# Optimization experiments

Measured on AMD Instinct MI355X. Metric: run time of the kernel, lower is better.

The kernel has to match this reference:

```python
import jax, jax.numpy as jnp
import numpy as np

D_MODEL = 768
HEAD_SIZE = 64

def setup_inputs() -> dict:
    key = jax.random.key(0)
    ks = jax.random.split(key, 7)
    B, S = 8, 2048
    x = jax.random.normal(ks[0], (B, S, D_MODEL), dtype=jnp.float32)
    s = 1.0 / np.sqrt(D_MODEL)
    Wq = jax.random.uniform(ks[1], (D_MODEL, HEAD_SIZE), jnp.float32, -s, s)
    bq = jnp.zeros((HEAD_SIZE,), jnp.float32)
    Wk = jax.random.uniform(ks[2], (D_MODEL, HEAD_SIZE), jnp.float32, -s, s)
    bk = jnp.zeros((HEAD_SIZE,), jnp.float32)
    Wv = jax.random.uniform(ks[3], (D_MODEL, HEAD_SIZE), jnp.float32, -s, s)
    bv = jnp.zeros((HEAD_SIZE,), jnp.float32)
    return {"x": x, "Wq": Wq, "bq": bq, "Wk": Wk, "bk": bk, "Wv": Wv, "bv": bv}

def reference(x, Wq, bq, Wk, bk, Wv, bv):
    # Single attention head: softmax(Q K^T / sqrt(head_size)) V
    q = jnp.einsum('bsd,dh->bsh', x, Wq) + bq  # [B,S,H]
    k = jnp.einsum('bsd,dh->bsh', x, Wk) + bk
    v = jnp.einsum('bsd,dh->bsh', x, Wv) + bv
    scale = 1.0 / jnp.sqrt(jnp.array(HEAD_SIZE, dtype=x.dtype))
    scores = jnp.einsum('bqh,bkh->bqk', q, k) * scale  # [B,S,S]
    attn = jax.nn.softmax(scores, axis=-1)
    out = jnp.einsum('bqk,bkh->bqh', attn, v)  # [B,S,H]
    return out
```

## Files before the change

kernel.cpp:

```cpp
#include <hip/hip_runtime.h>
#include <math.h>

#define D_MODEL 768
#define HS 64
#define BATCH 8
#define SEQ 2048
#define SCALE 0.125f
#define KSPLIT 8
#define KCHUNK (SEQ / KSPLIT)
#define PM 32

typedef _Float16 half_t;
typedef __attribute__((ext_vector_type(8))) _Float16 half8;
typedef __attribute__((ext_vector_type(4))) float floatx4;

typedef const __attribute__((address_space(1))) void gas_void;
typedef __attribute__((address_space(3))) void las_void;
__device__ __forceinline__ void gl_lds16(const void* g, void* l) {
    __builtin_amdgcn_global_load_lds((gas_void*)g, (las_void*)l, 16, 0, 0);
}
__device__ __forceinline__ void waitcnt_all() {
    __builtin_amdgcn_s_waitcnt(0);
}

__global__ __launch_bounds__(256)
void wconv_kernel(const float* __restrict__ Wq, const float* __restrict__ Wk,
                  const float* __restrict__ Wv, half_t* __restrict__ Wt)
{
    int m = blockIdx.x >> 6;
    int h = blockIdx.x & 63;
    const float* W = (m == 0) ? Wq : ((m == 1) ? Wk : Wv);
    half_t* dst = Wt + (size_t)blockIdx.x * D_MODEL;
    for (int k = threadIdx.x; k < D_MODEL; k += 256)
        dst[k] = (half_t)W[(size_t)k * HS + h];
}

__global__ __launch_bounds__(256)
void proj_kernel(const float* __restrict__ x, const half_t* __restrict__ Wt,
                 const float* __restrict__ bq, const float* __restrict__ bk,
                 const float* __restrict__ bv,
                 half_t* __restrict__ Qh, half_t* __restrict__ Kh,
                 half_t* __restrict__ Vt)
{
    __shared__ __align__(16) half_t xs[2][PM * 64];
    __shared__ __align__(16) half_t wt[2][192 * 64];

    const int tid = threadIdx.x;
    const int w = tid >> 6;
    const int lane = tid & 63;
    const int l15 = lane & 15;
    const int quad = lane >> 4;
    const long row0 = (long)blockIdx.x * PM;

    floatx4 acc[2][3];
#pragma unroll
    for (int i = 0; i < 2; ++i)
#pragma unroll
        for (int j = 0; j < 3; ++j) acc[i][j] = (floatx4){0.f, 0.f, 0.f, 0.f};

    float4 xA[2], xB[2];
    half8  wA[6], wB[6];

    auto loadx = [&](int k0, float4 (&v)[2]) {
        int r = tid >> 3, sc = tid & 7;
        int cg = sc ^ (r & 7);
        const float* p = x + (row0 + r) * D_MODEL + k0 + cg * 8;
        v[0] = *(const float4*)p;
        v[1] = *(const float4*)(p + 4);
    };
    auto loadw = [&](int k0, half8 (&wr)[6]) {
#pragma unroll
        for (int i = 0; i < 6; ++i) {
            int idx = i * 256 + tid;
            int r = idx >> 3, sc = idx & 7;
            int cg = sc ^ (r & 7);
            wr[i] = *(const half8*)(Wt + (size_t)r * D_MODEL + k0 + cg * 8);
        }
    };

    auto step = [&](int it, float4 (&xc)[2], half8 (&wc)[6],
                    float4 (&xn)[2], half8 (&wn)[6], int p) {
        {
            float4 a = xc[0], b = xc[1];
            half8 xh = (half8){(half_t)a.x, (half_t)a.y, (half_t)a.z, (half_t)a.w,
                               (half_t)b.x, (half_t)b.y, (half_t)b.z, (half_t)b.w};
            *(half8*)&xs[p][tid * 8] = xh;
        }
#pragma unroll
        for (int i = 0; i < 6; ++i)
            *(half8*)&wt[p][(i * 256 + tid) * 8] = wc[i];
        __syncthreads();
        int kn = (it + 1 < 12) ? (it + 1) * 64 : 0;
        loadx(kn, xn);
        loadw(kn, wn);
#pragma unroll
        for (int kst = 0; kst < 2; ++kst) {
            half8 af[2];
#pragma unroll
            for (int mt = 0; mt < 2; ++mt) {
                int r = mt * 16 + l15;
                int slot = (kst * 4 + quad) ^ (r & 7);
                af[mt] = *(const half8*)&xs[p][r * 64 + slot * 8];
            }
#pragma unroll
            for (int nt = 0; nt < 3; ++nt) {
                int r = w * 48 + nt * 16 + l15;
                int slot = (kst * 4 + quad) ^ (r & 7);
                half8 bf = *(const half8*)&wt[p][r * 64 + slot * 8];
#pragma unroll
                for (int mt = 0; mt < 2; ++mt)
                    acc[mt][nt] = __builtin_amdgcn_mfma_f32_16x16x32_f16(
                        af[mt], bf, acc[mt][nt], 0, 0, 0);
            }
        }
    };

    loadx(0, xA);
    loadw(0, wA);
#pragma unroll
    for (int it = 0; it < 12; it += 2) {
        step(it,     xA, wA, xB, wB, 0);
        step(it + 1, xB, wB, xA, wA, 1);
    }

#pragma unroll
    for (int nt = 0; nt < 3; ++nt) {
        int nbase = w * 48 + nt * 16;
        int mm = nbase >> 6;
        int h = (nbase + l15) & 63;
        const float* bias = (mm == 0) ? bq : ((mm == 1) ? bk : bv);
        float bval = bias[h];
#pragma unroll
        for (int mt = 0; mt < 2; ++mt)
#pragma unroll
            for (int r = 0; r < 4; ++r) {
                long R = row0 + mt * 16 + quad * 4 + r;
                half_t hv = (half_t)(acc[mt][nt][r] + bval);
                if (mm == 0)      Qh[R * HS + h] = hv;
                else if (mm == 1) Kh[R * HS + h] = hv;
                else {
                    long bb = R >> 11, s = R & 2047;
                    Vt[(bb * HS + h) * SEQ + s] = hv;
                }
            }
    }
}

__global__ __launch_bounds__(128)
void attn_kernel(const half_t* __restrict__ Qh, const half_t* __restrict__ Kh,
                 const half_t* __restrict__ Vt,
                 half_t* __restrict__ Opart, float* __restrict__ lpart)
{
    __shared__ __align__(16) half_t ks[2][64 * 64];
    __shared__ __align__(16) half_t vs[2][64 * 64];
    __shared__ __align__(16) half_t ps[2][16][72];

    const int tid = threadIdx.x;
    const int w = tid >> 6;
    const int lane = tid & 63;
    const int l15 = lane & 15;
    const int quad = lane >> 4;
    const int b = blockIdx.y;
    const int q0 = blockIdx.x * 128 + w * 64;
    const int kh = blockIdx.z;
    const int kk_begin = kh * KCHUNK;

    const half_t* Kb = Kh + (size_t)b * SEQ * HS;
    const half_t* Vb = Vt + (size_t)b * HS * SEQ;

    half8 qf[4][2];
#pragma unroll
    for (int mt = 0; mt < 4; ++mt)
#pragma unroll
        for (int kst = 0; kst < 2; ++kst) {
            half8 q = *(const half8*)(Qh + ((size_t)b * SEQ + q0 + mt * 16 + l15) * HS
                                      + kst * 32 + quad * 8);
#pragma unroll
            for (int j = 0; j < 8; ++j) q[j] = q[j] * (half_t)SCALE;
            qf[mt][kst] = q;
        }

    floatx4 oacc[4][4];
    float lsum[4][4];
#pragma unroll
    for (int mt = 0; mt < 4; ++mt) {
#pragma unroll
        for (int nt = 0; nt < 4; ++nt) oacc[mt][nt] = (floatx4){0.f, 0.f, 0.f, 0.f};
#pragma unroll
        for (int r = 0; r < 4; ++r) lsum[mt][r] = 0.f;
    }

    auto stage = [&](int p, int kk0) {
#pragma unroll
        for (int i = 0; i < 4; ++i) {
            int idx = i * 128 + tid;
            int r = idx >> 3, sc = idx & 7;
            int cg = sc ^ (r & 7);
            gl_lds16(Kb + (size_t)(kk0 + r) * HS + cg * 8, &ks[p][idx * 8]);
            gl_lds16(Vb + (size_t)r * SEQ + kk0 + cg * 8, &vs[p][idx * 8]);
        }
    };

    stage(0, kk_begin);

    for (int it = 0; it < KCHUNK / 64; ++it) {
        const int cur = it & 1;
        waitcnt_all();
        __syncthreads();
        if (it + 1 < KCHUNK / 64)
            stage(cur ^ 1, kk_begin + (it + 1) * 64);

        half8 vf[4][2];
#pragma unroll
        for (int nt = 0; nt < 4; ++nt)
#pragma unroll
            for (int kst = 0; kst < 2; ++kst) {
                int r = nt * 16 + l15;
                int slot = (kst * 4 + quad) ^ (r & 7);
                vf[nt][kst] = *(const half8*)&vs[cur][r * 64 + slot * 8];
            }

#pragma unroll
        for (int h2 = 0; h2 < 2; ++h2) {
            floatx4 sacc[2][4];
#pragma unroll
            for (int mtl = 0; mtl < 2; ++mtl)
#pragma unroll
                for (int nt = 0; nt < 4; ++nt) sacc[mtl][nt] = (floatx4){0.f, 0.f, 0.f, 0.f};
#pragma unroll
            for (int nt = 0; nt < 4; ++nt)
#pragma unroll
                for (int kst = 0; kst < 2; ++kst) {
                    int r = nt * 16 + l15;
                    int slot = (kst * 4 + quad) ^ (r & 7);
                    half8 kf = *(const half8*)&ks[cur][r * 64 + slot * 8];
#pragma unroll
                    for (int mtl = 0; mtl < 2; ++mtl)
                        sacc[mtl][nt] = __builtin_amdgcn_mfma_f32_16x16x32_f16(
                            qf[h2 * 2 + mtl][kst], kf, sacc[mtl][nt], 0, 0, 0);
                }

#pragma unroll
            for (int mtl = 0; mtl < 2; ++mtl) {
                int mt = h2 * 2 + mtl;
#pragma unroll
                for (int nt = 0; nt < 4; ++nt)
#pragma unroll
                    for (int r = 0; r < 4; ++r) {
                        float pv = __expf(sacc[mtl][nt][r]);
                        lsum[mt][r] += pv;
                        ps[w][quad * 4 + r][nt * 16 + l15] = (half_t)pv;
                    }
                half8 pfr[2];
#pragma unroll
                for (int kst = 0; kst < 2; ++kst)
                    pfr[kst] = *(const half8*)&ps[w][l15][kst * 32 + quad * 8];
#pragma unroll
                for (int nt = 0; nt < 4; ++nt)
#pragma unroll
                    for (int kst = 0; kst < 2; ++kst)
                        oacc[mt][nt] = __builtin_amdgcn_mfma_f32_16x16x32_f16(
                            pfr[kst], vf[nt][kst], oacc[mt][nt], 0, 0, 0);
            }
        }
    }

#pragma unroll
    for (int mt = 0; mt < 4; ++mt)
#pragma unroll
        for (int r = 0; r < 4; ++r) {
            float s = lsum[mt][r];
            s += __shfl_xor(s, 1);
            s += __shfl_xor(s, 2);
            s += __shfl_xor(s, 4);
            s += __shfl_xor(s, 8);
            lsum[mt][r] = s;
        }

    size_t obase = ((size_t)kh * BATCH + b) * SEQ * HS;
#pragma unroll
    for (int mt = 0; mt < 4; ++mt)
#pragma unroll
        for (int nt = 0; nt < 4; ++nt)
#pragma unroll
            for (int r = 0; r < 4; ++r) {
                int row = q0 + mt * 16 + quad * 4 + r;
                Opart[obase + (size_t)row * HS + nt * 16 + l15] = (half_t)oacc[mt][nt][r];
            }
    if (l15 == 0) {
#pragma unroll
        for (int mt = 0; mt < 4; ++mt)
#pragma unroll
            for (int r = 0; r < 4; ++r) {
                int row = q0 + mt * 16 + quad * 4 + r;
                lpart[((size_t)kh * BATCH + b) * SEQ + row] = lsum[mt][r];
            }
    }
}

__global__ __launch_bounds__(256)
void combine_kernel(const half_t* __restrict__ Opart, const float* __restrict__ lpart,
                    float* __restrict__ out)
{
    const size_t NT = (size_t)BATCH * SEQ * HS;
    const size_t BS = (size_t)BATCH * SEQ;
    size_t e0 = ((size_t)blockIdx.x * 256 + threadIdx.x) * 8;
    size_t row = e0 / HS;
    float o[8] = {0, 0, 0, 0, 0, 0, 0, 0};
    float l = 0.f;
#pragma unroll
    for (int i = 0; i < KSPLIT; ++i) {
        half8 oi = *(const half8*)(Opart + (size_t)i * NT + e0);
#pragma unroll
        for (int j = 0; j < 8; ++j) o[j] += (float)oi[j];
        l += lpart[(size_t)i * BS + row];
    }
    float inv = 1.f / l;
    float4 a = {o[0] * inv, o[1] * inv, o[2] * inv, o[3] * inv};
    float4 c = {o[4] * inv, o[5] * inv, o[6] * inv, o[7] * inv};
    *(float4*)(out + e0) = a;
    *(float4*)(out + e0 + 4) = c;
}

extern "C" void kernel_launch(void* const* d_in, const int* in_sizes, int n_in,
                              void* d_out, int out_size, void* d_ws, size_t ws_size,
                              hipStream_t stream) {
    const float* x  = (const float*)d_in[0];
    const float* Wq = (const float*)d_in[1];
    const float* bq = (const float*)d_in[2];
    const float* Wk = (const float*)d_in[3];
    const float* bk = (const float*)d_in[4];
    const float* Wv = (const float*)d_in[5];
    const float* bv = (const float*)d_in[6];
    float* out = (float*)d_out;

    const size_t per = (size_t)BATCH * SEQ * HS;
    half_t* Qh = (half_t*)d_ws;
    half_t* Kh = Qh + per;
    half_t* Vt = Kh + per;
    half_t* Wt = Vt + per;
    half_t* Opart = Wt + 3 * HS * D_MODEL;
    float*  lpart = (float*)(Opart + (size_t)KSPLIT * per);

    wconv_kernel<<<dim3(3 * HS), dim3(256), 0, stream>>>(Wq, Wk, Wv, Wt);
    proj_kernel<<<dim3(BATCH * SEQ / PM), dim3(256), 0, stream>>>(
        x, Wt, bq, bk, bv, Qh, Kh, Vt);
    attn_kernel<<<dim3(SEQ / 128, BATCH, KSPLIT), dim3(128), 0, stream>>>(
        Qh, Kh, Vt, Opart, lpart);
    combine_kernel<<<dim3((BATCH * SEQ * HS) / (256 * 8)), dim3(256), 0, stream>>>(
        Opart, lpart, out);
}
```

Measured before the change: 135.5 us.

## Split projection output columns across blocks and use four waves per attention block

The projection kernel now splits the 192 output columns into two halves handled by separate blocks. That doubles the grid and halves each block's weight tile and register footprint, but x is now loaded and converted twice. The attention kernel moves from 2 waves of 64 query rows to 4 waves of 32 query rows per block, so each block still covers 128 queries while per-wave registers drop and the K/V staging is shared by more waves. Launch-bound occupancy hints are added to both kernels to raise waves per CU and improve latency hiding.

```diff
diff --git a/kernel.cpp b/kernel.cpp
--- a/kernel.cpp
+++ b/kernel.cpp
@@ -9,6 +9,7 @@
 #define KSPLIT 8
 #define KCHUNK (SEQ / KSPLIT)
 #define PM 32
+#define PN 96
 
 typedef _Float16 half_t;
 typedef __attribute__((ext_vector_type(8))) _Float16 half8;
@@ -35,7 +36,7 @@
         dst[k] = (half_t)W[(size_t)k * HS + h];
 }
 
-__global__ __launch_bounds__(256)
+__global__ __launch_bounds__(256, 4)
 void proj_kernel(const float* __restrict__ x, const half_t* __restrict__ Wt,
                  const float* __restrict__ bq, const float* __restrict__ bk,
                  const float* __restrict__ bv,
@@ -43,23 +44,24 @@
                  half_t* __restrict__ Vt)
 {
     __shared__ __align__(16) half_t xs[2][PM * 64];
-    __shared__ __align__(16) half_t wt[2][192 * 64];
+    __shared__ __align__(16) half_t wtl[2][PN * 64];
 
     const int tid = threadIdx.x;
     const int w = tid >> 6;
     const int lane = tid & 63;
     const int l15 = lane & 15;
     const int quad = lane >> 4;
-    const long row0 = (long)blockIdx.x * PM;
-
-    floatx4 acc[2][3];
-#pragma unroll
-    for (int i = 0; i < 2; ++i)
-#pragma unroll
-        for (int j = 0; j < 3; ++j) acc[i][j] = (floatx4){0.f, 0.f, 0.f, 0.f};
+    const int nhalf = blockIdx.x & 1;
+    const long row0 = (long)(blockIdx.x >> 1) * PM;
+    const int msub = w >> 1;
+    const int nsub = w & 1;
+
+    floatx4 acc[3];
+#pragma unroll
+    for (int j = 0; j < 3; ++j) acc[j] = (floatx4){0.f, 0.f, 0.f, 0.f};
 
     float4 xA[2], xB[2];
-    half8  wA[6], wB[6];
+    half8  wA[3], wB[3];
 
     auto loadx = [&](int k0, float4 (&v)[2]) {
         int r = tid >> 3, sc = tid & 7;
@@ -68,18 +70,18 @@
         v[0] = *(const float4*)p;
         v[1] = *(const float4*)(p + 4);
     };
-    auto loadw = [&](int k0, half8 (&wr)[6]) {
-#pragma unroll
-        for (int i = 0; i < 6; ++i) {
+    auto loadw = [&](int k0, half8 (&wr)[3]) {
+#pragma unroll
+        for (int i = 0; i < 3; ++i) {
             int idx = i * 256 + tid;
             int r = idx >> 3, sc = idx & 7;
             int cg = sc ^ (r & 7);
-            wr[i] = *(const half8*)(Wt + (size_t)r * D_MODEL + k0 + cg * 8);
+            wr[i] = *(const half8*)(Wt + (size_t)(nhalf * PN + r) * D_MODEL + k0 + cg * 8);
         }
     };
 
-    auto step = [&](int it, float4 (&xc)[2], half8 (&wc)[6],
-                    float4 (&xn)[2], half8 (&wn)[6], int p) {
+    auto step = [&](int it, float4 (&xc)[2], half8 (&wc)[3],
+                    float4 (&xn)[2], half8 (&wn)[3], int p) {
         {
             float4 a = xc[0], b = xc[1];
             half8 xh = (half8){(half_t)a.x, (half_t)a.y, (half_t)a.z, (half_t)a.w,
@@ -87,30 +89,24 @@
             *(half8*)&xs[p][tid * 8] = xh;
         }
 #pragma unroll
-        for (int i = 0; i < 6; ++i)
-            *(half8*)&wt[p][(i * 256 + tid) * 8] = wc[i];
+        for (int i = 0; i < 3; ++i)
+            *(half8*)&wtl[p][(i * 256 + tid) * 8] = wc[i];
         __syncthreads();
         int kn = (it + 1 < 12) ? (it + 1) * 64 : 0;
         loadx(kn, xn);
         loadw(kn, wn);
 #pragma unroll
         for (int kst = 0; kst < 2; ++kst) {
-            half8 af[2];
-#pragma unroll
-            for (int mt = 0; mt < 2; ++mt) {
-                int r = mt * 16 + l15;
-                int slot = (kst * 4 + quad) ^ (r & 7);
-                af[mt] = *(const half8*)&xs[p][r * 64 + slot * 8];
-            }
+            int ra = msub * 16 + l15;
+            int slota = (kst * 4 + quad) ^ (ra & 7);
+            half8 af = *(const half8*)&xs[p][ra * 64 + slota * 8];
 #pragma unroll
             for (int nt = 0; nt < 3; ++nt) {
-                int r = w * 48 + nt * 16 + l15;
-                int slot = (kst * 4 + quad) ^ (r & 7);
-                half8 bf = *(const half8*)&wt[p][r * 64 + slot * 8];
-#pragma unroll
-                for (int mt = 0; mt < 2; ++mt)
-                    acc[mt][nt] = __builtin_amdgcn_mfma_f32_16x16x32_f16(
-                        af[mt], bf, acc[mt][nt], 0, 0, 0);
+                int rb = nsub * 48 + nt * 16 + l15;
+                int slotb = (kst * 4 + quad) ^ (rb & 7);
+                half8 bf = *(const half8*)&wtl[p][rb * 64 + slotb * 8];
+                acc[nt] = __builtin_amdgcn_mfma_f32_16x16x32_f16(
+                    af, bf, acc[nt], 0, 0, 0);
             }
         }
     };
@@ -125,35 +121,33 @@
 
 #pragma unroll
     for (int nt = 0; nt < 3; ++nt) {
-        int nbase = w * 48 + nt * 16;
+        int nbase = nhalf * PN + nsub * 48 + nt * 16;
         int mm = nbase >> 6;
         int h = (nbase + l15) & 63;
         const float* bias = (mm == 0) ? bq : ((mm == 1) ? bk : bv);
         float bval = bias[h];
 #pragma unroll
-        for (int mt = 0; mt < 2; ++mt)
-#pragma unroll
-            for (int r = 0; r < 4; ++r) {
-                long R = row0 + mt * 16 + quad * 4 + r;
-                half_t hv = (half_t)(acc[mt][nt][r] + bval);
-                if (mm == 0)      Qh[R * HS + h] = hv;
-                else if (mm == 1) Kh[R * HS + h] = hv;
-                else {
-                    long bb = R >> 11, s = R & 2047;
-                    Vt[(bb * HS + h) * SEQ + s] = hv;
-                }
-            }
-    }
-}
-
-__global__ __launch_bounds__(128)
+        for (int r = 0; r < 4; ++r) {
+            long R = row0 + msub * 16 + quad * 4 + r;
+            half_t hv = (half_t)(acc[nt][r] + bval);
+            if (mm == 0)      Qh[R * HS + h] = hv;
+            else if (mm == 1) Kh[R * HS + h] = hv;
+            else {
+                long bb = R >> 11, s = R & 2047;
+                Vt[(bb * HS + h) * SEQ + s] = hv;
+            }
+        }
+    }
+}
+
+__global__ __launch_bounds__(256, 3)
 void attn_kernel(const half_t* __restrict__ Qh, const half_t* __restrict__ Kh,
                  const half_t* __restrict__ Vt,
                  half_t* __restrict__ Opart, float* __restrict__ lpart)
 {
     __shared__ __align__(16) half_t ks[2][64 * 64];
     __shared__ __align__(16) half_t vs[2][64 * 64];
-    __shared__ __align__(16) half_t ps[2][16][72];
+    __shared__ __align__(16) half_t ps[4][16][72];
 
     const int tid = threadIdx.x;
     const int w = tid >> 6;
@@ -161,16 +155,16 @@
     const int l15 = lane & 15;
     const int quad = lane >> 4;
     const int b = blockIdx.y;
-    const int q0 = blockIdx.x * 128 + w * 64;
+    const int q0 = blockIdx.x * 128 + w * 32;
     const int kh = blockIdx.z;
     const int kk_begin = kh * KCHUNK;
 
     const half_t* Kb = Kh + (size_t)b * SEQ * HS;
     const half_t* Vb = Vt + (size_t)b * HS * SEQ;
 
-    half8 qf[4][2];
-#pragma unroll
-    for (int mt = 0; mt < 4; ++mt)
+    half8 qf[2][2];
+#pragma unroll
+    for (int mt = 0; mt < 2; ++mt)
 #pragma unroll
         for (int kst = 0; kst < 2; ++kst) {
             half8 q = *(const half8*)(Qh + ((size_t)b * SEQ + q0 + mt * 16 + l15) * HS
@@ -180,10 +174,10 @@
             qf[mt][kst] = q;
         }
 
-    floatx4 oacc[4][4];
-    float lsum[4][4];
-#pragma unroll
-    for (int mt = 0; mt < 4; ++mt) {
+    floatx4 oacc[2][4];
+    float lsum[2][4];
+#pragma unroll
+    for (int mt = 0; mt < 2; ++mt) {
 #pragma unroll
         for (int nt = 0; nt < 4; ++nt) oacc[mt][nt] = (floatx4){0.f, 0.f, 0.f, 0.f};
 #pragma unroll
@@ -192,8 +186,8 @@
 
     auto stage = [&](int p, int kk0) {
 #pragma unroll
-        for (int i = 0; i < 4; ++i) {
-            int idx = i * 128 + tid;
+        for (int i = 0; i < 2; ++i) {
+            int idx = i * 256 + tid;
             int r = idx >> 3, sc = idx & 7;
             int cg = sc ^ (r & 7);
             gl_lds16(Kb + (size_t)(kk0 + r) * HS + cg * 8, &ks[p][idx * 8]);
@@ -220,53 +214,49 @@
                 vf[nt][kst] = *(const half8*)&vs[cur][r * 64 + slot * 8];
             }
 
-#pragma unroll
-        for (int h2 = 0; h2 < 2; ++h2) {
-            floatx4 sacc[2][4];
-#pragma unroll
-            for (int mtl = 0; mtl < 2; ++mtl)
-#pragma unroll
-                for (int nt = 0; nt < 4; ++nt) sacc[mtl][nt] = (floatx4){0.f, 0.f, 0.f, 0.f};
+        floatx4 sacc[2][4];
+#pragma unroll
+        for (int mt = 0; mt < 2; ++mt)
+#pragma unroll
+            for (int nt = 0; nt < 4; ++nt) sacc[mt][nt] = (floatx4){0.f, 0.f, 0.f, 0.f};
+#pragma unroll
+        for (int nt = 0; nt < 4; ++nt)
+#pragma unroll
+            for (int kst = 0; kst < 2; ++kst) {
+                int r = nt * 16 + l15;
+                int slot = (kst * 4 + quad) ^ (r & 7);
+                half8 kf = *(const half8*)&ks[cur][r * 64 + slot * 8];
+#pragma unroll
+                for (int mt = 0; mt < 2; ++mt)
+                    sacc[mt][nt] = __builtin_amdgcn_mfma_f32_16x16x32_f16(
+                        qf[mt][kst], kf, sacc[mt][nt], 0, 0, 0);
+            }
+
+#pragma unroll
+        for (int mt = 0; mt < 2; ++mt) {
 #pragma unroll
             for (int nt = 0; nt < 4; ++nt)
 #pragma unroll
-                for (int kst = 0; kst < 2; ++kst) {
-                    int r = nt * 16 + l15;
-                    int slot = (kst * 4 + quad) ^ (r & 7);
-                    half8 kf = *(const half8*)&ks[cur][r * 64 + slot * 8];
-#pragma unroll
-                    for (int mtl = 0; mtl < 2; ++mtl)
-                        sacc[mtl][nt] = __builtin_amdgcn_mfma_f32_16x16x32_f16(
-                            qf[h2 * 2 + mtl][kst], kf, sacc[mtl][nt], 0, 0, 0);
+                for (int r = 0; r < 4; ++r) {
+                    float pv = __expf(sacc[mt][nt][r]);
+                    lsum[mt][r] += pv;
+                    ps[w][quad * 4 + r][nt * 16 + l15] = (half_t)pv;
                 }
-
-#pragma unroll
-            for (int mtl = 0; mtl < 2; ++mtl) {
-                int mt = h2 * 2 + mtl;
-#pragma unroll
-                for (int nt = 0; nt < 4; ++nt)
-#pragma unroll
-                    for (int r = 0; r < 4; ++r) {
-                        float pv = __expf(sacc[mtl][nt][r]);
-                        lsum[mt][r] += pv;
-                        ps[w][quad * 4 + r][nt * 16 + l15] = (half_t)pv;
-                    }
-                half8 pfr[2];
+            half8 pfr[2];
+#pragma unroll
+            for (int kst = 0; kst < 2; ++kst)
+                pfr[kst] = *(const half8*)&ps[w][l15][kst * 32 + quad * 8];
+#pragma unroll
+            for (int nt = 0; nt < 4; ++nt)
 #pragma unroll
                 for (int kst = 0; kst < 2; ++kst)
-                    pfr[kst] = *(const half8*)&ps[w][l15][kst * 32 + quad * 8];
-#pragma unroll
-                for (int nt = 0; nt < 4; ++nt)
-#pragma unroll
-                    for (int kst = 0; kst < 2; ++kst)
-                        oacc[mt][nt] = __builtin_amdgcn_mfma_f32_16x16x32_f16(
-                            pfr[kst], vf[nt][kst], oacc[mt][nt], 0, 0, 0);
-            }
-        }
-    }
-
-#pragma unroll
-    for (int mt = 0; mt < 4; ++mt)
+                    oacc[mt][nt] = __builtin_amdgcn_mfma_f32_16x16x32_f16(
+                        pfr[kst], vf[nt][kst], oacc[mt][nt], 0, 0, 0);
+        }
+    }
+
+#pragma unroll
+    for (int mt = 0; mt < 2; ++mt)
 #pragma unroll
         for (int r = 0; r < 4; ++r) {
             float s = lsum[mt][r];
@@ -279,7 +269,7 @@
 
     size_t obase = ((size_t)kh * BATCH + b) * SEQ * HS;
 #pragma unroll
-    for (int mt = 0; mt < 4; ++mt)
+    for (int mt = 0; mt < 2; ++mt)
 #pragma unroll
         for (int nt = 0; nt < 4; ++nt)
 #pragma unroll
@@ -289,7 +279,7 @@
             }
     if (l15 == 0) {
 #pragma unroll
-        for (int mt = 0; mt < 4; ++mt)
+        for (int mt = 0; mt < 2; ++mt)
 #pragma unroll
             for (int r = 0; r < 4; ++r) {
                 int row = q0 + mt * 16 + quad * 4 + r;
@@ -343,9 +333,9 @@
     float*  lpart = (float*)(Opart + (size_t)KSPLIT * per);
 
     wconv_kernel<<<dim3(3 * HS), dim3(256), 0, stream>>>(Wq, Wk, Wv, Wt);
-    proj_kernel<<<dim3(BATCH * SEQ / PM), dim3(256), 0, stream>>>(
+    proj_kernel<<<dim3((BATCH * SEQ / PM) * 2), dim3(256), 0, stream>>>(
         x, Wt, bq, bk, bv, Qh, Kh, Vt);
-    attn_kernel<<<dim3(SEQ / 128, BATCH, KSPLIT), dim3(128), 0, stream>>>(
+    attn_kernel<<<dim3(SEQ / 128, BATCH, KSPLIT), dim3(256), 0, stream>>>(
         Qh, Kh, Vt, Opart, lpart);
     combine_kernel<<<dim3((BATCH * SEQ * HS) / (256 * 8)), dim3(256), 0, stream>>>(
         Opart, lpart, out);
```

Measured after the change: 153.3 us. +13.1%, slower.
